# Optimization experiments

Measured on AMD Instinct MI355X. Metric: run time of the kernel, lower is better.

The kernel has to match this reference:

```python
import jax, jax.numpy as jnp
import numpy as np

B = 64          # batch
NV = 256        # n_vert per rod
CS = [256, 256] # cs_n_vert
N = 3 * NV      # num_nodes
RBC = [100, 200]  # rigid_body_coupling_index
HID = 128


def _build_adjacency():
    A = np.zeros((N, N), dtype=np.float32)
    # chain edges: parent rod, child1 rod, child2 rod (hop=1)
    for i in range(NV - 1):
        A[i, i + 1] = 1; A[i + 1, i] = 1
    for i in range(NV, NV + CS[0] - 1):
        A[i, i + 1] = 1; A[i + 1, i] = 1
    for i in range(2 * NV, 2 * NV + CS[1] - 1):
        A[i, i + 1] = 1; A[i + 1, i] = 1
    zero_mask = np.all(A == 0, axis=-1).astype(np.float32)  # (N,)
    A = (A + np.eye(N, dtype=np.float32)) * (1.0 - zero_mask)  # broadcast over columns, as in torch
    # rigid-body coupling edges (asymmetric, faithful to the source)
    for i, r in enumerate(RBC):
        base = NV * (i + 1)
        A[base, r - 1] = 1; A[base, r] = 1; A[base, r + 1] = 1
        if i == 0:
            A[r, NV] = 1; A[r, NV + 1] = 1
        else:
            A[r, NV + CS[i - 1]] = 1; A[r, NV + CS[i - 1] + 1] = 1
    return A


def setup_inputs() -> dict:
    key = jax.random.key(0)
    ks = jax.random.split(key, 10)
    dims = [(6, 2 * HID), (2 * HID, HID), (HID, HID), (HID, 3)]  # gcn1..gcn4
    params = {}
    for li, (fi, fo) in enumerate(dims):
        params[f"W{li+1}"] = jax.random.normal(ks[li], (fo, fi), jnp.float32) / np.sqrt(fi)
        params[f"b{li+1}"] = jnp.zeros((fo,), jnp.float32)
    return {
        "x": jax.random.normal(ks[8], (B, N, 6), jnp.float32),
        "inputs": jax.random.normal(ks[9], (B, N, 3), jnp.float32),
        "adjacency": jnp.asarray(_build_adjacency()),
        **params,
        "parent_sel": jnp.array([0, NV - 1], jnp.int32),
        "child1_sel": jnp.array([NV - 1], jnp.int32),
        "child2_sel": jnp.array([NV - 1], jnp.int32),
    }


def _gcn(A_norm, x, W, b):
    # linear then symmetric-normalized dense aggregation
    return jnp.einsum('ij,bjf->bif', A_norm, x @ W.T + b)


def reference(x, inputs, adjacency, W1, b1, W2, b2, W3, b3, W4, b4,
              parent_sel, child1_sel, child2_sel):
    deg = adjacency.sum(axis=-1)
    deg_safe = jnp.where(deg == 0, 1.0, deg)
    d = jnp.where(deg == 0, 0.0, deg_safe ** -0.5)
    A_norm = adjacency * d[:, None] * d[None, :]

    x4 = x.reshape(B, 3, NV, -1)
    in4 = inputs.reshape(B, 3, NV, 3)
    # clamp input positions (first 3 features) at grasped vertices
    x4 = x4.at[:, 0, parent_sel, 0:3].set(in4[:, 0, parent_sel])
    x4 = x4.at[:, 1, child1_sel, 0:3].set(in4[:, 1, child1_sel])
    x4 = x4.at[:, 2, child2_sel, 0:3].set(in4[:, 2, child2_sel])
    h = x4.reshape(B, N, -1)

    h = jax.nn.relu(_gcn(A_norm, h, W1, b1))
    h = jax.nn.relu(_gcn(A_norm, h, W2, b2))
    h = _gcn(A_norm, h, W3, b3)
    out = _gcn(A_norm, h, W4, b4)

    o4 = out.reshape(B, 3, NV, 3)
    o4 = o4.at[:, 0, parent_sel].set(in4[:, 0, parent_sel])
    o4 = o4.at[:, 1, child1_sel].set(in4[:, 1, child1_sel])
    o4 = o4.at[:, 2, child2_sel].set(in4[:, 2, child2_sel])
    return o4.reshape(B, N, 3)
```

## Files before the change

### kernel.cpp

```cpp
#include <hip/hip_runtime.h>
#include <math.h>

#define B_ 64
#define NV_ 256
#define N_ 768
#define NNZ 8
#define M_ (B_ * N_)

typedef unsigned short us8 __attribute__((ext_vector_type(8)));
typedef unsigned short us4 __attribute__((ext_vector_type(4)));
typedef __bf16 bf16x8 __attribute__((ext_vector_type(8)));
typedef float f32x4 __attribute__((ext_vector_type(4)));

__device__ inline float bf2f(unsigned short u) {
    return __uint_as_float(((unsigned int)u) << 16);
}
__device__ inline unsigned short f2bf(float f) {
    unsigned int u = __float_as_uint(f);
    unsigned int r = u + 0x7fffu + ((u >> 16) & 1u);
    return (unsigned short)(r >> 16);
}
__device__ inline bf16x8 ld_bf8(const unsigned short* p) {
    us8 u = *(const us8*)p;
    return __builtin_bit_cast(bf16x8, u);
}


__global__ __launch_bounds__(256) void k_deg_conv(
    const float* __restrict__ A, const float* __restrict__ W2,
    const float* __restrict__ W3, const int* __restrict__ psel, int np,
    const int* __restrict__ c1, int n1, const int* __restrict__ c2, int n2,
    float* __restrict__ dinv, int* __restrict__ clampf,
    unsigned short* __restrict__ W2b, unsigned short* __restrict__ W3b) {
    int blk = blockIdx.x, tid = threadIdx.x;
    if (blk < 192) {
        int wave = tid >> 6, lane = tid & 63;
        int i = blk * 4 + wave;
        float deg = 0.f;
#pragma unroll
        for (int c0 = 0; c0 < N_; c0 += 64) deg += A[(size_t)i * N_ + c0 + lane];
#pragma unroll
        for (int o = 32; o > 0; o >>= 1) deg += __shfl_xor(deg, o);
        if (lane == 0) dinv[i] = (deg == 0.f) ? 0.f : 1.0f / sqrtf(deg);
    } else if (blk < 384) {
        int idx = (blk - 192) * 256 + tid;
        if (idx < 128 * 256) W2b[idx] = f2bf(W2[idx]);
        else W3b[idx - 128 * 256] = f2bf(W3[idx - 128 * 256]);
    } else {
        clampf[tid] = 0;
        clampf[tid + 256] = 0;
        clampf[tid + 512] = 0;
        __syncthreads();
        if (tid < np) clampf[psel[tid]] = 1;
        else if (tid - np < n1) clampf[NV_ + c1[tid - np]] = 1;
        else if (tid - np - n1 < n2) clampf[2 * NV_ + c2[tid - np - n1]] = 1;
    }
}


__global__ __launch_bounds__(256) void k_sparse(const float* __restrict__ A,
                                                const float* __restrict__ dinv,
                                                int* __restrict__ cols,
                                                float* __restrict__ vals,
                                                float* __restrict__ rowsum) {
    __shared__ int wc[4][NNZ];
    __shared__ float wa[4][NNZ];
    int wave = threadIdx.x >> 6, lane = threadIdx.x & 63;
    int i = blockIdx.x * 4 + wave;
    float di = dinv[i];
    int cnt = 0;
    float rs = 0.f;
#pragma unroll
    for (int c0 = 0; c0 < N_; c0 += 64) {
        int c = c0 + lane;
        float a = A[(size_t)i * N_ + c];
        unsigned long long m = __ballot(a != 0.f);
        if (a != 0.f) {
            float v = a * di * dinv[c];
            int pos = cnt + __popcll(m & ((1ull << lane) - 1ull));
            if (pos < NNZ) {
                wc[wave][pos] = c;
                wa[wave][pos] = v;
            }
            rs += v;
        }
        cnt += (int)__popcll(m);
    }
#pragma unroll
    for (int o = 32; o > 0; o >>= 1) rs += __shfl_xor(rs, o);
    __syncthreads();
    int nn = cnt < NNZ ? cnt : NNZ;
    if (lane < NNZ) {
        int c = (lane < nn) ? wc[wave][lane] : i;
        float v = (lane < nn) ? wa[wave][lane] : 0.f;
        cols[i * NNZ + lane] = c;
        vals[i * NNZ + lane] = v;
    }
    if (lane == 0) rowsum[i] = rs;
}


__global__ __launch_bounds__(256) void k_layer12(
    const float* __restrict__ x, const float* __restrict__ inputs,
    const int* __restrict__ cols, const float* __restrict__ vals,
    const int* __restrict__ clampf, const float* __restrict__ rowsum,
    const float* __restrict__ W1, const float* __restrict__ b1,
    const unsigned short* __restrict__ W2b, const float* __restrict__ b2,
    unsigned short* __restrict__ T2) {
    __shared__ float Xs[64][6];
    __shared__ float W1T[6][256];
    __shared__ float b1s[256];

    int tid = threadIdx.x;
    int blk = blockIdx.x;
    int i0 = (blk % 12) * 64;
    int base = (blk / 12) * N_;
    int wave = tid >> 6, lane = tid & 63;
    int lrow = lane & 15, kgrp = lane >> 4;

    for (int t = tid; t < 1536; t += 256) {
        int k = t >> 8, c = t & 255;
        W1T[k][c] = W1[c * 6 + k];
    }
    b1s[tid] = b1[tid];

    for (int t = lane; t < 96; t += 64) {
        int f = t % 6, ro = t / 6;
        int i = i0 + wave * 16 + ro;
        float s = 0.f;
#pragma unroll
        for (int k = 0; k < NNZ; ++k) {
            int c = cols[i * NNZ + k];
            float v = vals[i * NNZ + k];
            float val = (f < 3 && clampf[c]) ? inputs[(size_t)(base + c) * 3 + f]
                                             : x[(size_t)(base + c) * 6 + f];
            s += v * val;
        }
        Xs[wave * 16 + ro][f] = s;
    }
    __syncthreads();

    int i = i0 + wave * 16 + lrow;
    size_t g = (size_t)(base + i);
    float rs = rowsum[i];
    float xa[6];
#pragma unroll
    for (int k = 0; k < 6; ++k) xa[k] = Xs[wave * 16 + lrow][k];

    f32x4 acc[8];
#pragma unroll
    for (int j = 0; j < 8; ++j) acc[j] = (f32x4){0.f, 0.f, 0.f, 0.f};

#pragma unroll
    for (int s = 0; s < 8; ++s) {
        int c0 = s * 32 + kgrp * 8;
        float h[8];
        f32x4 bv0 = *(const f32x4*)&b1s[c0];
        f32x4 bv1 = *(const f32x4*)&b1s[c0 + 4];
#pragma unroll
        for (int e = 0; e < 4; ++e) {
            h[e] = rs * bv0[e];
            h[4 + e] = rs * bv1[e];
        }
#pragma unroll
        for (int k = 0; k < 6; ++k) {
            f32x4 w0 = *(const f32x4*)&W1T[k][c0];
            f32x4 w1 = *(const f32x4*)&W1T[k][c0 + 4];
#pragma unroll
            for (int e = 0; e < 4; ++e) {
                h[e] += xa[k] * w0[e];
                h[4 + e] += xa[k] * w1[e];
            }
        }
        us8 o;
#pragma unroll
        for (int e = 0; e < 8; ++e) o[e] = f2bf(fmaxf(h[e], 0.f));
        bf16x8 af = __builtin_bit_cast(bf16x8, o);
#pragma unroll
        for (int j = 0; j < 8; ++j) {
            bf16x8 w = ld_bf8(W2b + (size_t)(j * 16 + lrow) * 256 + c0);
            acc[j] = __builtin_amdgcn_mfma_f32_16x16x32_bf16(w, af, acc[j], 0, 0, 0);
        }
    }

#pragma unroll
    for (int j = 0; j < 8; ++j) {
        f32x4 bv = *(const f32x4*)&b2[j * 16 + kgrp * 4];
        us4 o;
#pragma unroll
        for (int e = 0; e < 4; ++e) o[e] = f2bf(acc[j][e] + bv[e]);
        *(us4*)(T2 + g * 128 + j * 16 + kgrp * 4) = o;
    }
}


__global__ __launch_bounds__(256) void k_layer3s(
    const unsigned short* __restrict__ T2, const int* __restrict__ cols,
    const float* __restrict__ vals, const unsigned short* __restrict__ W3b,
    const float* __restrict__ b3, const float* __restrict__ W4,
    float* __restrict__ S) {
    __shared__ float W4s[128 * 3];

    int tid = threadIdx.x;
    int blk = blockIdx.x;
    int i0 = (blk % 12) * 64;
    int base = (blk / 12) * N_;
    int wave = tid >> 6, lane = tid & 63;
    int lrow = lane & 15, kgrp = lane >> 4;

    for (int t = tid; t < 384; t += 256) {
        int d = t % 3, nfeat = t / 3;
        W4s[t] = W4[d * 128 + nfeat];
    }
    __syncthreads();

    int i = i0 + wave * 16 + lrow;
    size_t g = (size_t)(base + i);

    float fa[4][8];
#pragma unroll
    for (int s = 0; s < 4; ++s)
#pragma unroll
        for (int e = 0; e < 8; ++e) fa[s][e] = 0.f;

#pragma unroll
    for (int k = 0; k < NNZ; ++k) {
        int c = cols[i * NNZ + k];
        float v = vals[i * NNZ + k];
        const unsigned short* p = T2 + (size_t)(base + c) * 128 + kgrp * 8;
#pragma unroll
        for (int s = 0; s < 4; ++s) {
            us8 z = *(const us8*)(p + s * 32);
#pragma unroll
            for (int e = 0; e < 8; ++e) fa[s][e] += v * bf2f(z[e]);
        }
    }

    bf16x8 af[4];
#pragma unroll
    for (int s = 0; s < 4; ++s) {
        us8 o;
#pragma unroll
        for (int e = 0; e < 8; ++e) o[e] = f2bf(fmaxf(fa[s][e], 0.f));
        af[s] = __builtin_bit_cast(bf16x8, o);
    }

    f32x4 acc[8];
#pragma unroll
    for (int j = 0; j < 8; ++j) acc[j] = (f32x4){0.f, 0.f, 0.f, 0.f};
#pragma unroll
    for (int s = 0; s < 4; ++s) {
#pragma unroll
        for (int j = 0; j < 8; ++j) {
            bf16x8 w = ld_bf8(W3b + (size_t)(j * 16 + lrow) * 128 + s * 32 + kgrp * 8);
            acc[j] = __builtin_amdgcn_mfma_f32_16x16x32_bf16(w, af[s], acc[j], 0, 0, 0);
        }
    }

    float s0 = 0.f, s1 = 0.f, s2 = 0.f;
#pragma unroll
    for (int j = 0; j < 8; ++j) {
        f32x4 bv = *(const f32x4*)&b3[j * 16 + kgrp * 4];
#pragma unroll
        for (int e = 0; e < 4; ++e) {
            float tv = acc[j][e] + bv[e];
            int nfeat = j * 16 + kgrp * 4 + e;
            s0 += tv * W4s[nfeat * 3 + 0];
            s1 += tv * W4s[nfeat * 3 + 1];
            s2 += tv * W4s[nfeat * 3 + 2];
        }
    }
    s0 += __shfl_xor(s0, 16); s0 += __shfl_xor(s0, 32);
    s1 += __shfl_xor(s1, 16); s1 += __shfl_xor(s1, 32);
    s2 += __shfl_xor(s2, 16); s2 += __shfl_xor(s2, 32);
    if (kgrp == 0) {
        S[g * 3 + 0] = s0;
        S[g * 3 + 1] = s1;
        S[g * 3 + 2] = s2;
    }
}


__global__ __launch_bounds__(256) void k_out2(const float* __restrict__ S,
                                              const float* __restrict__ inputs,
                                              const int* __restrict__ cols,
                                              const float* __restrict__ vals,
                                              const float* __restrict__ rowsum,
                                              const float* __restrict__ b4,
                                              const int* __restrict__ clampf,
                                              float* __restrict__ out) {
    int idx = blockIdx.x * 256 + threadIdx.x;
    if (idx >= M_ * 3) return;
    int f = idx % 3;
    int r = idx / 3;
    int i = r % N_;
    int base = r - i;
    if (clampf[i]) {
        out[idx] = inputs[(size_t)r * 3 + f];
        return;
    }
    float s = rowsum[i] * b4[f];
#pragma unroll
    for (int k = 0; k < NNZ; ++k) {
        int c = cols[i * NNZ + k];
        float vik = vals[i * NNZ + k];
        float u = 0.f;
#pragma unroll
        for (int p = 0; p < NNZ; ++p) {
            int j = cols[c * NNZ + p];
            u += vals[c * NNZ + p] * S[(size_t)(base + j) * 3 + f];
        }
        s += vik * u;
    }
    out[idx] = s;
}


extern "C" void kernel_launch(void* const* d_in, const int* in_sizes, int n_in,
                              void* d_out, int out_size, void* d_ws, size_t ws_size,
                              hipStream_t stream) {
    const float* x      = (const float*)d_in[0];
    const float* inputs = (const float*)d_in[1];
    const float* A      = (const float*)d_in[2];
    const float* W1     = (const float*)d_in[3];
    const float* b1     = (const float*)d_in[4];
    const float* W2     = (const float*)d_in[5];
    const float* b2     = (const float*)d_in[6];
    const float* W3     = (const float*)d_in[7];
    const float* b3     = (const float*)d_in[8];
    const float* W4     = (const float*)d_in[9];
    const float* b4     = (const float*)d_in[10];
    const int* psel     = (const int*)d_in[11];
    const int* c1sel    = (const int*)d_in[12];
    const int* c2sel    = (const int*)d_in[13];
    int np = in_sizes[11], n1 = in_sizes[12], n2 = in_sizes[13];
    float* out = (float*)d_out;

    char* ws = (char*)d_ws;
    float* dinv            = (float*)(ws + 0);
    float* rowsum          = (float*)(ws + 3072);
    int*   clampf          = (int*)(ws + 9216);
    int*   cols            = (int*)(ws + 12288);
    float* vals            = (float*)(ws + 61440);
    unsigned short* W2b    = (unsigned short*)(ws + 110592);
    unsigned short* W3b    = (unsigned short*)(ws + 176128);
    float* S               = (float*)(ws + 417792);
    unsigned short* T2     = (unsigned short*)(ws + 27144192);

    k_deg_conv<<<385, 256, 0, stream>>>(A, W2, W3, psel, np, c1sel, n1, c2sel, n2,
                                        dinv, clampf, W2b, W3b);
    k_sparse<<<192, 256, 0, stream>>>(A, dinv, cols, vals, rowsum);

    k_layer12<<<M_ / 64, 256, 0, stream>>>(x, inputs, cols, vals, clampf, rowsum,
                                           W1, b1, W2b, b2, T2);
    k_layer3s<<<M_ / 64, 256, 0, stream>>>(T2, cols, vals, W3b, b3, W4, S);
    k_out2<<<(M_ * 3 + 255) / 256, 256, 0, stream>>>(S, inputs, cols, vals,
                                                     rowsum, b4, clampf, out);
}
```

Baseline: 75.44 us.

## Fuse all stages into one persistent kernel with grid-wide barriers

Merges the five separate kernel launches into one persistent kernel that walks virtual blocks and separates stages with atomic-counter grid barriers. The degree and sparse-extraction passes are also merged so A is read once, with normalization applied in a later small pass. The aim is to remove launch overhead and inter-kernel gaps. In exchange it adds global-barrier spin costs, a memset launch, and an occupancy query on the host per call. The barrier has a timeout fallback that could silently break correctness if the grid is not fully co-resident.

New measurement: 153.2 us. 2.03x slower.

```diff
diff --git a/kernel.cpp b/kernel.cpp
--- a/kernel.cpp
+++ b/kernel.cpp
@@ -25,335 +25,334 @@
     return __builtin_bit_cast(bf16x8, u);
 }
 
-
-__global__ __launch_bounds__(256) void k_deg_conv(
-    const float* __restrict__ A, const float* __restrict__ W2,
-    const float* __restrict__ W3, const int* __restrict__ psel, int np,
-    const int* __restrict__ c1, int n1, const int* __restrict__ c2, int n2,
-    float* __restrict__ dinv, int* __restrict__ clampf,
-    unsigned short* __restrict__ W2b, unsigned short* __restrict__ W3b) {
-    int blk = blockIdx.x, tid = threadIdx.x;
-    if (blk < 192) {
-        int wave = tid >> 6, lane = tid & 63;
-        int i = blk * 4 + wave;
-        float deg = 0.f;
-#pragma unroll
-        for (int c0 = 0; c0 < N_; c0 += 64) deg += A[(size_t)i * N_ + c0 + lane];
-#pragma unroll
-        for (int o = 32; o > 0; o >>= 1) deg += __shfl_xor(deg, o);
-        if (lane == 0) dinv[i] = (deg == 0.f) ? 0.f : 1.0f / sqrtf(deg);
-    } else if (blk < 384) {
-        int idx = (blk - 192) * 256 + tid;
-        if (idx < 128 * 256) W2b[idx] = f2bf(W2[idx]);
-        else W3b[idx - 128 * 256] = f2bf(W3[idx - 128 * 256]);
-    } else {
-        clampf[tid] = 0;
-        clampf[tid + 256] = 0;
-        clampf[tid + 512] = 0;
-        __syncthreads();
-        if (tid < np) clampf[psel[tid]] = 1;
-        else if (tid - np < n1) clampf[NV_ + c1[tid - np]] = 1;
-        else if (tid - np - n1 < n2) clampf[2 * NV_ + c2[tid - np - n1]] = 1;
-    }
-}
-
-
-__global__ __launch_bounds__(256) void k_sparse(const float* __restrict__ A,
-                                                const float* __restrict__ dinv,
-                                                int* __restrict__ cols,
-                                                float* __restrict__ vals,
-                                                float* __restrict__ rowsum) {
-    __shared__ int wc[4][NNZ];
-    __shared__ float wa[4][NNZ];
-    int wave = threadIdx.x >> 6, lane = threadIdx.x & 63;
-    int i = blockIdx.x * 4 + wave;
-    float di = dinv[i];
-    int cnt = 0;
-    float rs = 0.f;
-#pragma unroll
-    for (int c0 = 0; c0 < N_; c0 += 64) {
-        int c = c0 + lane;
-        float a = A[(size_t)i * N_ + c];
-        unsigned long long m = __ballot(a != 0.f);
-        if (a != 0.f) {
-            float v = a * di * dinv[c];
-            int pos = cnt + __popcll(m & ((1ull << lane) - 1ull));
-            if (pos < NNZ) {
-                wc[wave][pos] = c;
-                wa[wave][pos] = v;
-            }
-            rs += v;
-        }
-        cnt += (int)__popcll(m);
-    }
-#pragma unroll
-    for (int o = 32; o > 0; o >>= 1) rs += __shfl_xor(rs, o);
+struct GP {
+    const float *x, *inputs, *A, *W1, *b1, *W2, *b2, *W3, *b3, *W4, *b4;
+    const int *psel, *c1s, *c2s;
+    int np, n1, n2;
+    float* dinv;
+    float* rowsum;
+    int* clampf;
+    int* cols;
+    float* vals;
+    unsigned short* W2b;
+    unsigned short* W3b;
+    float* S;
+    unsigned short* T2;
+    unsigned int* bar;
+    float* out;
+};
+
+__device__ __forceinline__ void gsync(unsigned int* bar, int slot) {
     __syncthreads();
-    int nn = cnt < NNZ ? cnt : NNZ;
-    if (lane < NNZ) {
-        int c = (lane < nn) ? wc[wave][lane] : i;
-        float v = (lane < nn) ? wa[wave][lane] : 0.f;
-        cols[i * NNZ + lane] = c;
-        vals[i * NNZ + lane] = v;
-    }
-    if (lane == 0) rowsum[i] = rs;
-}
-
-
-__global__ __launch_bounds__(256) void k_layer12(
-    const float* __restrict__ x, const float* __restrict__ inputs,
-    const int* __restrict__ cols, const float* __restrict__ vals,
-    const int* __restrict__ clampf, const float* __restrict__ rowsum,
-    const float* __restrict__ W1, const float* __restrict__ b1,
-    const unsigned short* __restrict__ W2b, const float* __restrict__ b2,
-    unsigned short* __restrict__ T2) {
-    __shared__ float Xs[64][6];
-    __shared__ float W1T[6][256];
-    __shared__ float b1s[256];
-
-    int tid = threadIdx.x;
-    int blk = blockIdx.x;
-    int i0 = (blk % 12) * 64;
-    int base = (blk / 12) * N_;
+    if (threadIdx.x == 0) {
+        __threadfence();
+        atomicAdd(&bar[slot], 1u);
+        unsigned int nb = gridDim.x;
+        long long t0 = clock64();
+        while (atomicAdd(&bar[slot], 0u) < nb) {
+            __builtin_amdgcn_s_sleep(16);
+            if (clock64() - t0 > 200000000LL) break;
+        }
+        __threadfence();
+    }
+    __syncthreads();
+}
+
+__global__ __launch_bounds__(256) void k_mega(GP p) {
+    int tid = threadIdx.x, blk = blockIdx.x;
+    int gd = gridDim.x;
     int wave = tid >> 6, lane = tid & 63;
     int lrow = lane & 15, kgrp = lane >> 4;
 
+    __shared__ union {
+        struct { int wc[4][NNZ]; float wa[4][NNZ]; } sp;
+        struct { float Xs[64][6]; float W1T[6][256]; float b1s[256]; } l12;
+        struct { float W4s[384]; } l3;
+    } sm;
+
+    for (int vb = blk; vb < 385; vb += gd) {
+        if (vb < 192) {
+            int i = vb * 4 + wave;
+            float deg = 0.f;
+            int cnt = 0;
+#pragma unroll
+            for (int c0 = 0; c0 < N_; c0 += 64) {
+                float a = p.A[(size_t)i * N_ + c0 + lane];
+                deg += a;
+                unsigned long long m = __ballot(a != 0.f);
+                if (a != 0.f) {
+                    int pos = cnt + __popcll(m & ((1ull << lane) - 1ull));
+                    if (pos < NNZ) {
+                        sm.sp.wc[wave][pos] = c0 + lane;
+                        sm.sp.wa[wave][pos] = a;
+                    }
+                }
+                cnt += (int)__popcll(m);
+            }
+#pragma unroll
+            for (int o = 32; o > 0; o >>= 1) deg += __shfl_xor(deg, o);
+            __syncthreads();
+            int nn = cnt < NNZ ? cnt : NNZ;
+            if (lane < NNZ) {
+                p.cols[i * NNZ + lane] = (lane < nn) ? sm.sp.wc[wave][lane] : i;
+                p.vals[i * NNZ + lane] = (lane < nn) ? sm.sp.wa[wave][lane] : 0.f;
+            }
+            if (lane == 0) p.dinv[i] = (deg == 0.f) ? 0.f : 1.0f / sqrtf(deg);
+        } else if (vb < 384) {
+            int idx = (vb - 192) * 256 + tid;
+            if (idx < 32768) p.W2b[idx] = f2bf(p.W2[idx]);
+            else p.W3b[idx - 32768] = f2bf(p.W3[idx - 32768]);
+        } else {
+            p.clampf[tid] = 0;
+            p.clampf[tid + 256] = 0;
+            p.clampf[tid + 512] = 0;
+            __syncthreads();
+            if (tid < p.np) p.clampf[p.psel[tid]] = 1;
+            else if (tid - p.np < p.n1) p.clampf[NV_ + p.c1s[tid - p.np]] = 1;
+            else if (tid - p.np - p.n1 < p.n2)
+                p.clampf[2 * NV_ + p.c2s[tid - p.np - p.n1]] = 1;
+        }
+        __syncthreads();
+    }
+    gsync(p.bar, 0);
+
+    for (int idx = blk * 256 + tid; idx < N_ * NNZ; idx += gd * 256) {
+        int i = idx >> 3;
+        int c = p.cols[idx];
+        float v = p.vals[idx] * p.dinv[i] * p.dinv[c];
+        p.vals[idx] = v;
+        float rs = v;
+        rs += __shfl_xor(rs, 1);
+        rs += __shfl_xor(rs, 2);
+        rs += __shfl_xor(rs, 4);
+        if ((idx & 7) == 0) p.rowsum[i] = rs;
+    }
+    gsync(p.bar, 1);
+
     for (int t = tid; t < 1536; t += 256) {
         int k = t >> 8, c = t & 255;
-        W1T[k][c] = W1[c * 6 + k];
-    }
-    b1s[tid] = b1[tid];
-
-    for (int t = lane; t < 96; t += 64) {
-        int f = t % 6, ro = t / 6;
-        int i = i0 + wave * 16 + ro;
-        float s = 0.f;
-#pragma unroll
-        for (int k = 0; k < NNZ; ++k) {
-            int c = cols[i * NNZ + k];
-            float v = vals[i * NNZ + k];
-            float val = (f < 3 && clampf[c]) ? inputs[(size_t)(base + c) * 3 + f]
-                                             : x[(size_t)(base + c) * 6 + f];
-            s += v * val;
-        }
-        Xs[wave * 16 + ro][f] = s;
-    }
-    __syncthreads();
-
-    int i = i0 + wave * 16 + lrow;
-    size_t g = (size_t)(base + i);
-    float rs = rowsum[i];
-    float xa[6];
-#pragma unroll
-    for (int k = 0; k < 6; ++k) xa[k] = Xs[wave * 16 + lrow][k];
-
-    f32x4 acc[8];
-#pragma unroll
-    for (int j = 0; j < 8; ++j) acc[j] = (f32x4){0.f, 0.f, 0.f, 0.f};
-
-#pragma unroll
-    for (int s = 0; s < 8; ++s) {
-        int c0 = s * 32 + kgrp * 8;
-        float h[8];
-        f32x4 bv0 = *(const f32x4*)&b1s[c0];
-        f32x4 bv1 = *(const f32x4*)&b1s[c0 + 4];
-#pragma unroll
-        for (int e = 0; e < 4; ++e) {
-            h[e] = rs * bv0[e];
-            h[4 + e] = rs * bv1[e];
-        }
-#pragma unroll
-        for (int k = 0; k < 6; ++k) {
-            f32x4 w0 = *(const f32x4*)&W1T[k][c0];
-            f32x4 w1 = *(const f32x4*)&W1T[k][c0 + 4];
+        sm.l12.W1T[k][c] = p.W1[c * 6 + k];
+    }
+    sm.l12.b1s[tid] = p.b1[tid];
+
+    for (int vb = blk; vb < 768; vb += gd) {
+        int i0 = (vb % 12) * 64;
+        int base = (vb / 12) * N_;
+        __syncthreads();
+
+        for (int t = lane; t < 96; t += 64) {
+            int f = t % 6, ro = t / 6;
+            int i = i0 + wave * 16 + ro;
+            float s = 0.f;
+#pragma unroll
+            for (int k = 0; k < NNZ; ++k) {
+                int c = p.cols[i * NNZ + k];
+                float v = p.vals[i * NNZ + k];
+                float val = (f < 3 && p.clampf[c]) ? p.inputs[(size_t)(base + c) * 3 + f]
+                                                   : p.x[(size_t)(base + c) * 6 + f];
+                s += v * val;
+            }
+            sm.l12.Xs[wave * 16 + ro][f] = s;
+        }
+        __syncthreads();
+
+        int i = i0 + wave * 16 + lrow;
+        size_t g = (size_t)(base + i);
+        float rs = p.rowsum[i];
+        float xa[6];
+#pragma unroll
+        for (int k = 0; k < 6; ++k) xa[k] = sm.l12.Xs[wave * 16 + lrow][k];
+
+        f32x4 acc[8];
+#pragma unroll
+        for (int j = 0; j < 8; ++j) acc[j] = (f32x4){0.f, 0.f, 0.f, 0.f};
+
+#pragma unroll
+        for (int s = 0; s < 8; ++s) {
+            int c0 = s * 32 + kgrp * 8;
+            float h[8];
+            f32x4 bv0 = *(const f32x4*)&sm.l12.b1s[c0];
+            f32x4 bv1 = *(const f32x4*)&sm.l12.b1s[c0 + 4];
 #pragma unroll
             for (int e = 0; e < 4; ++e) {
-                h[e] += xa[k] * w0[e];
-                h[4 + e] += xa[k] * w1[e];
-            }
-        }
-        us8 o;
-#pragma unroll
-        for (int e = 0; e < 8; ++e) o[e] = f2bf(fmaxf(h[e], 0.f));
-        bf16x8 af = __builtin_bit_cast(bf16x8, o);
+                h[e] = rs * bv0[e];
+                h[4 + e] = rs * bv1[e];
+            }
+#pragma unroll
+            for (int k = 0; k < 6; ++k) {
+                f32x4 w0 = *(const f32x4*)&sm.l12.W1T[k][c0];
+                f32x4 w1 = *(const f32x4*)&sm.l12.W1T[k][c0 + 4];
+#pragma unroll
+                for (int e = 0; e < 4; ++e) {
+                    h[e] += xa[k] * w0[e];
+                    h[4 + e] += xa[k] * w1[e];
+                }
+            }
+            us8 o;
+#pragma unroll
+            for (int e = 0; e < 8; ++e) o[e] = f2bf(fmaxf(h[e], 0.f));
+            bf16x8 af = __builtin_bit_cast(bf16x8, o);
+#pragma unroll
+            for (int j = 0; j < 8; ++j) {
+                bf16x8 w = ld_bf8(p.W2b + (size_t)(j * 16 + lrow) * 256 + c0);
+                acc[j] = __builtin_amdgcn_mfma_f32_16x16x32_bf16(w, af, acc[j], 0, 0, 0);
+            }
+        }
+
 #pragma unroll
         for (int j = 0; j < 8; ++j) {
-            bf16x8 w = ld_bf8(W2b + (size_t)(j * 16 + lrow) * 256 + c0);
-            acc[j] = __builtin_amdgcn_mfma_f32_16x16x32_bf16(w, af, acc[j], 0, 0, 0);
-        }
-    }
-
-#pragma unroll
-    for (int j = 0; j < 8; ++j) {
-        f32x4 bv = *(const f32x4*)&b2[j * 16 + kgrp * 4];
-        us4 o;
-#pragma unroll
-        for (int e = 0; e < 4; ++e) o[e] = f2bf(acc[j][e] + bv[e]);
-        *(us4*)(T2 + g * 128 + j * 16 + kgrp * 4) = o;
-    }
-}
-
-
-__global__ __launch_bounds__(256) void k_layer3s(
-    const unsigned short* __restrict__ T2, const int* __restrict__ cols,
-    const float* __restrict__ vals, const unsigned short* __restrict__ W3b,
-    const float* __restrict__ b3, const float* __restrict__ W4,
-    float* __restrict__ S) {
-    __shared__ float W4s[128 * 3];
-
-    int tid = threadIdx.x;
-    int blk = blockIdx.x;
-    int i0 = (blk % 12) * 64;
-    int base = (blk / 12) * N_;
-    int wave = tid >> 6, lane = tid & 63;
-    int lrow = lane & 15, kgrp = lane >> 4;
+            f32x4 bv = *(const f32x4*)&p.b2[j * 16 + kgrp * 4];
+            us4 o;
+#pragma unroll
+            for (int e = 0; e < 4; ++e) o[e] = f2bf(acc[j][e] + bv[e]);
+            *(us4*)(p.T2 + g * 128 + j * 16 + kgrp * 4) = o;
+        }
+    }
+    gsync(p.bar, 2);
 
     for (int t = tid; t < 384; t += 256) {
         int d = t % 3, nfeat = t / 3;
-        W4s[t] = W4[d * 128 + nfeat];
+        sm.l3.W4s[t] = p.W4[d * 128 + nfeat];
     }
     __syncthreads();
 
-    int i = i0 + wave * 16 + lrow;
-    size_t g = (size_t)(base + i);
-
-    float fa[4][8];
-#pragma unroll
-    for (int s = 0; s < 4; ++s)
-#pragma unroll
-        for (int e = 0; e < 8; ++e) fa[s][e] = 0.f;
-
-#pragma unroll
-    for (int k = 0; k < NNZ; ++k) {
-        int c = cols[i * NNZ + k];
-        float v = vals[i * NNZ + k];
-        const unsigned short* p = T2 + (size_t)(base + c) * 128 + kgrp * 8;
+    for (int vb = blk; vb < 768; vb += gd) {
+        int i0 = (vb % 12) * 64;
+        int base = (vb / 12) * N_;
+        int i = i0 + wave * 16 + lrow;
+        size_t g = (size_t)(base + i);
+
+        float fa[4][8];
+#pragma unroll
+        for (int s = 0; s < 4; ++s)
+#pragma unroll
+            for (int e = 0; e < 8; ++e) fa[s][e] = 0.f;
+
+#pragma unroll
+        for (int k = 0; k < NNZ; ++k) {
+            int c = p.cols[i * NNZ + k];
+            float v = p.vals[i * NNZ + k];
+            const unsigned short* pt = p.T2 + (size_t)(base + c) * 128 + kgrp * 8;
+#pragma unroll
+            for (int s = 0; s < 4; ++s) {
+                us8 z = *(const us8*)(pt + s * 32);
+#pragma unroll
+                for (int e = 0; e < 8; ++e) fa[s][e] += v * bf2f(z[e]);
+            }
+        }
+
+        bf16x8 af[4];
 #pragma unroll
         for (int s = 0; s < 4; ++s) {
-            us8 z = *(const us8*)(p + s * 32);
-#pragma unroll
-            for (int e = 0; e < 8; ++e) fa[s][e] += v * bf2f(z[e]);
-        }
-    }
-
-    bf16x8 af[4];
-#pragma unroll
-    for (int s = 0; s < 4; ++s) {
-        us8 o;
-#pragma unroll
-        for (int e = 0; e < 8; ++e) o[e] = f2bf(fmaxf(fa[s][e], 0.f));
-        af[s] = __builtin_bit_cast(bf16x8, o);
-    }
-
-    f32x4 acc[8];
-#pragma unroll
-    for (int j = 0; j < 8; ++j) acc[j] = (f32x4){0.f, 0.f, 0.f, 0.f};
-#pragma unroll
-    for (int s = 0; s < 4; ++s) {
+            us8 o;
+#pragma unroll
+            for (int e = 0; e < 8; ++e) o[e] = f2bf(fmaxf(fa[s][e], 0.f));
+            af[s] = __builtin_bit_cast(bf16x8, o);
+        }
+
+        f32x4 acc[8];
+#pragma unroll
+        for (int j = 0; j < 8; ++j) acc[j] = (f32x4){0.f, 0.f, 0.f, 0.f};
+#pragma unroll
+        for (int s = 0; s < 4; ++s) {
+#pragma unroll
+            for (int j = 0; j < 8; ++j) {
+                bf16x8 w = ld_bf8(p.W3b + (size_t)(j * 16 + lrow) * 128 + s * 32 + kgrp * 8);
+                acc[j] = __builtin_amdgcn_mfma_f32_16x16x32_bf16(w, af[s], acc[j], 0, 0, 0);
+            }
+        }
+
+        float s0 = 0.f, s1 = 0.f, s2 = 0.f;
 #pragma unroll
         for (int j = 0; j < 8; ++j) {
-            bf16x8 w = ld_bf8(W3b + (size_t)(j * 16 + lrow) * 128 + s * 32 + kgrp * 8);
-            acc[j] = __builtin_amdgcn_mfma_f32_16x16x32_bf16(w, af[s], acc[j], 0, 0, 0);
-        }
-    }
-
-    float s0 = 0.f, s1 = 0.f, s2 = 0.f;
-#pragma unroll
-    for (int j = 0; j < 8; ++j) {
-        f32x4 bv = *(const f32x4*)&b3[j * 16 + kgrp * 4];
-#pragma unroll
-        for (int e = 0; e < 4; ++e) {
-            float tv = acc[j][e] + bv[e];
-            int nfeat = j * 16 + kgrp * 4 + e;
-            s0 += tv * W4s[nfeat * 3 + 0];
-            s1 += tv * W4s[nfeat * 3 + 1];
-            s2 += tv * W4s[nfeat * 3 + 2];
-        }
-    }
-    s0 += __shfl_xor(s0, 16); s0 += __shfl_xor(s0, 32);
-    s1 += __shfl_xor(s1, 16); s1 += __shfl_xor(s1, 32);
-    s2 += __shfl_xor(s2, 16); s2 += __shfl_xor(s2, 32);
-    if (kgrp == 0) {
-        S[g * 3 + 0] = s0;
-        S[g * 3 + 1] = s1;
-        S[g * 3 + 2] = s2;
-    }
-}
-
-
-__global__ __launch_bounds__(256) void k_out2(const float* __restrict__ S,
-                                              const float* __restrict__ inputs,
-                                              const int* __restrict__ cols,
-                                              const float* __restrict__ vals,
-                                              const float* __restrict__ rowsum,
-                                              const float* __restrict__ b4,
-                                              const int* __restrict__ clampf,
-                                              float* __restrict__ out) {
-    int idx = blockIdx.x * 256 + threadIdx.x;
-    if (idx >= M_ * 3) return;
-    int f = idx % 3;
-    int r = idx / 3;
-    int i = r % N_;
-    int base = r - i;
-    if (clampf[i]) {
-        out[idx] = inputs[(size_t)r * 3 + f];
-        return;
-    }
-    float s = rowsum[i] * b4[f];
-#pragma unroll
-    for (int k = 0; k < NNZ; ++k) {
-        int c = cols[i * NNZ + k];
-        float vik = vals[i * NNZ + k];
-        float u = 0.f;
-#pragma unroll
-        for (int p = 0; p < NNZ; ++p) {
-            int j = cols[c * NNZ + p];
-            u += vals[c * NNZ + p] * S[(size_t)(base + j) * 3 + f];
-        }
-        s += vik * u;
-    }
-    out[idx] = s;
+            f32x4 bv = *(const f32x4*)&p.b3[j * 16 + kgrp * 4];
+#pragma unroll
+            for (int e = 0; e < 4; ++e) {
+                float tv = acc[j][e] + bv[e];
+                int nfeat = j * 16 + kgrp * 4 + e;
+                s0 += tv * sm.l3.W4s[nfeat * 3 + 0];
+                s1 += tv * sm.l3.W4s[nfeat * 3 + 1];
+                s2 += tv * sm.l3.W4s[nfeat * 3 + 2];
+            }
+        }
+        s0 += __shfl_xor(s0, 16); s0 += __shfl_xor(s0, 32);
+        s1 += __shfl_xor(s1, 16); s1 += __shfl_xor(s1, 32);
+        s2 += __shfl_xor(s2, 16); s2 += __shfl_xor(s2, 32);
+        if (kgrp == 0) {
+            p.S[g * 3 + 0] = s0;
+            p.S[g * 3 + 1] = s1;
+            p.S[g * 3 + 2] = s2;
+        }
+    }
+    gsync(p.bar, 3);
+
+    for (int idx = blk * 256 + tid; idx < M_ * 3; idx += gd * 256) {
+        int f = idx % 3;
+        int r = idx / 3;
+        int i = r % N_;
+        int base = r - i;
+        if (p.clampf[i]) {
+            p.out[idx] = p.inputs[(size_t)r * 3 + f];
+        } else {
+            float s = p.rowsum[i] * p.b4[f];
+#pragma unroll
+            for (int k = 0; k < NNZ; ++k) {
+                int c = p.cols[i * NNZ + k];
+                float vik = p.vals[i * NNZ + k];
+                float u = 0.f;
+#pragma unroll
+                for (int q = 0; q < NNZ; ++q) {
+                    int j = p.cols[c * NNZ + q];
+                    u += p.vals[c * NNZ + q] * p.S[(size_t)(base + j) * 3 + f];
+                }
+                s += vik * u;
+            }
+            p.out[idx] = s;
+        }
+    }
 }
 
 
 extern "C" void kernel_launch(void* const* d_in, const int* in_sizes, int n_in,
                               void* d_out, int out_size, void* d_ws, size_t ws_size,
                               hipStream_t stream) {
-    const float* x      = (const float*)d_in[0];
-    const float* inputs = (const float*)d_in[1];
-    const float* A      = (const float*)d_in[2];
-    const float* W1     = (const float*)d_in[3];
-    const float* b1     = (const float*)d_in[4];
-    const float* W2     = (const float*)d_in[5];
-    const float* b2     = (const float*)d_in[6];
-    const float* W3     = (const float*)d_in[7];
-    const float* b3     = (const float*)d_in[8];
-    const float* W4     = (const float*)d_in[9];
-    const float* b4     = (const float*)d_in[10];
-    const int* psel     = (const int*)d_in[11];
-    const int* c1sel    = (const int*)d_in[12];
-    const int* c2sel    = (const int*)d_in[13];
-    int np = in_sizes[11], n1 = in_sizes[12], n2 = in_sizes[13];
-    float* out = (float*)d_out;
-
     char* ws = (char*)d_ws;
-    float* dinv            = (float*)(ws + 0);
-    float* rowsum          = (float*)(ws + 3072);
-    int*   clampf          = (int*)(ws + 9216);
-    int*   cols            = (int*)(ws + 12288);
-    float* vals            = (float*)(ws + 61440);
-    unsigned short* W2b    = (unsigned short*)(ws + 110592);
-    unsigned short* W3b    = (unsigned short*)(ws + 176128);
-    float* S               = (float*)(ws + 417792);
-    unsigned short* T2     = (unsigned short*)(ws + 27144192);
-
-    k_deg_conv<<<385, 256, 0, stream>>>(A, W2, W3, psel, np, c1sel, n1, c2sel, n2,
-                                        dinv, clampf, W2b, W3b);
-    k_sparse<<<192, 256, 0, stream>>>(A, dinv, cols, vals, rowsum);
-
-    k_layer12<<<M_ / 64, 256, 0, stream>>>(x, inputs, cols, vals, clampf, rowsum,
-                                           W1, b1, W2b, b2, T2);
-    k_layer3s<<<M_ / 64, 256, 0, stream>>>(T2, cols, vals, W3b, b3, W4, S);
-    k_out2<<<(M_ * 3 + 255) / 256, 256, 0, stream>>>(S, inputs, cols, vals,
-                                                     rowsum, b4, clampf, out);
-}
+    GP p;
+    p.x      = (const float*)d_in[0];
+    p.inputs = (const float*)d_in[1];
+    p.A      = (const float*)d_in[2];
+    p.W1     = (const float*)d_in[3];
+    p.b1     = (const float*)d_in[4];
+    p.W2     = (const float*)d_in[5];
+    p.b2     = (const float*)d_in[6];
+    p.W3     = (const float*)d_in[7];
+    p.b3     = (const float*)d_in[8];
+    p.W4     = (const float*)d_in[9];
+    p.b4     = (const float*)d_in[10];
+    p.psel   = (const int*)d_in[11];
+    p.c1s    = (const int*)d_in[12];
+    p.c2s    = (const int*)d_in[13];
+    p.np = in_sizes[11];
+    p.n1 = in_sizes[12];
+    p.n2 = in_sizes[13];
+    p.dinv   = (float*)(ws + 0);
+    p.rowsum = (float*)(ws + 3072);
+    p.clampf = (int*)(ws + 9216);
+    p.cols   = (int*)(ws + 12288);
+    p.vals   = (float*)(ws + 61440);
+    p.W2b    = (unsigned short*)(ws + 110592);
+    p.W3b    = (unsigned short*)(ws + 176128);
+    p.bar    = (unsigned int*)(ws + 212992);
+    p.S      = (float*)(ws + 417792);
+    p.T2     = (unsigned short*)(ws + 27144192);
+    p.out    = (float*)d_out;
+
+    int bpc = 0;
+    hipError_t e = hipOccupancyMaxActiveBlocksPerMultiprocessor(&bpc, k_mega, 256, 0);
+    if (e != hipSuccess || bpc < 1) bpc = 1;
+    int grid = bpc * 256;
+    if (grid > 768) grid = 768;
+
+    hipMemsetAsync(p.bar, 0, 16, stream);
+    k_mega<<<grid, 256, 0, stream>>>(p);
+}
```

## Fuse layers 1-3 with halo recompute in LDS, split final aggregation

Applied to the files above, without the earlier changes.

Merges the layer-1/2 and layer-3 kernels into one kernel. Each block recomputes layer-2 features for its 64 rows plus a halo of neighbour rows (up to 80 slots) and keeps them in shared memory, so the bf16 T2 intermediate never makes a global round trip. The final two-hop aggregation is split into two one-hop kernels through a small U buffer, which avoids the 64 nested gathers per output. In exchange, halo rows add redundant MFMA work, one wave runs an extra pass, LDS use grows, and there is one more kernel launch. Halo slots are capped at 80, and neighbours beyond that fall back to slot 0.

After: 88.39 us. 1.17x slower.

```diff
diff --git a/kernel.cpp b/kernel.cpp
--- a/kernel.cpp
+++ b/kernel.cpp
@@ -6,6 +6,8 @@
 #define N_ 768
 #define NNZ 8
 #define M_ (B_ * N_)
+#define NH 80
+#define TP 136
 
 typedef unsigned short us8 __attribute__((ext_vector_type(8)));
 typedef unsigned short us4 __attribute__((ext_vector_type(4)));
@@ -44,8 +46,8 @@
         if (lane == 0) dinv[i] = (deg == 0.f) ? 0.f : 1.0f / sqrtf(deg);
     } else if (blk < 384) {
         int idx = (blk - 192) * 256 + tid;
-        if (idx < 128 * 256) W2b[idx] = f2bf(W2[idx]);
-        else W3b[idx - 128 * 256] = f2bf(W3[idx - 128 * 256]);
+        if (idx < 32768) W2b[idx] = f2bf(W2[idx]);
+        else W3b[idx - 32768] = f2bf(W3[idx - 32768]);
     } else {
         clampf[tid] = 0;
         clampf[tid + 256] = 0;
@@ -91,42 +93,76 @@
     __syncthreads();
     int nn = cnt < NNZ ? cnt : NNZ;
     if (lane < NNZ) {
-        int c = (lane < nn) ? wc[wave][lane] : i;
-        float v = (lane < nn) ? wa[wave][lane] : 0.f;
-        cols[i * NNZ + lane] = c;
-        vals[i * NNZ + lane] = v;
+        cols[i * NNZ + lane] = (lane < nn) ? wc[wave][lane] : i;
+        vals[i * NNZ + lane] = (lane < nn) ? wa[wave][lane] : 0.f;
     }
     if (lane == 0) rowsum[i] = rs;
 }
 
 
-__global__ __launch_bounds__(256) void k_layer12(
+__global__ __launch_bounds__(256) void k_l123(
     const float* __restrict__ x, const float* __restrict__ inputs,
     const int* __restrict__ cols, const float* __restrict__ vals,
     const int* __restrict__ clampf, const float* __restrict__ rowsum,
     const float* __restrict__ W1, const float* __restrict__ b1,
     const unsigned short* __restrict__ W2b, const float* __restrict__ b2,
-    unsigned short* __restrict__ T2) {
-    __shared__ float Xs[64][6];
+    const unsigned short* __restrict__ W3b, const float* __restrict__ b3,
+    const float* __restrict__ W4, float* __restrict__ S) {
+    __shared__ unsigned short T2L[NH][TP];
+    __shared__ float Xs[NH][6];
     __shared__ float W1T[6][256];
     __shared__ float b1s[256];
-
-    int tid = threadIdx.x;
-    int blk = blockIdx.x;
+    __shared__ float W4s[384];
+    __shared__ short lmap[N_];
+    __shared__ int ilist[NH];
+    __shared__ int nhs;
+
+    int tid = threadIdx.x, blk = blockIdx.x;
     int i0 = (blk % 12) * 64;
     int base = (blk / 12) * N_;
     int wave = tid >> 6, lane = tid & 63;
     int lrow = lane & 15, kgrp = lane >> 4;
 
+    for (int t = tid; t < N_; t += 256) lmap[t] = -1;
+    if (tid == 0) nhs = 66;
     for (int t = tid; t < 1536; t += 256) {
         int k = t >> 8, c = t & 255;
         W1T[k][c] = W1[c * 6 + k];
     }
     b1s[tid] = b1[tid];
-
-    for (int t = lane; t < 96; t += 64) {
-        int f = t % 6, ro = t / 6;
-        int i = i0 + wave * 16 + ro;
+    for (int t = tid; t < 384; t += 256) {
+        int d = t % 3, nf = t / 3;
+        W4s[t] = W4[d * 128 + nf];
+    }
+    __syncthreads();
+    for (int t = tid; t < 66; t += 256) {
+        int c = i0 - 1 + t;
+        if (c >= 0 && c < N_) {
+            lmap[c] = (short)t;
+            ilist[t] = c;
+        } else {
+            ilist[t] = i0;
+        }
+    }
+    __syncthreads();
+    for (int t = tid; t < 64 * NNZ; t += 256) {
+        int i = i0 + (t >> 3);
+        int c = cols[i * NNZ + (t & 7)];
+        if (lmap[c] < 0) {
+            int slot = atomicAdd(&nhs, 1);
+            if (slot < NH) {
+                lmap[c] = (short)slot;
+                ilist[slot] = c;
+            }
+        }
+    }
+    __syncthreads();
+    int NHs = nhs;
+    if (NHs > NH) NHs = NH;
+
+    for (int t = tid; t < NHs * 6; t += 256) {
+        int sl = t / 6, f = t % 6;
+        int i = ilist[sl];
         float s = 0.f;
 #pragma unroll
         for (int k = 0; k < NNZ; ++k) {
@@ -136,159 +172,170 @@
                                              : x[(size_t)(base + c) * 6 + f];
             s += v * val;
         }
-        Xs[wave * 16 + ro][f] = s;
-    }
-    __syncthreads();
-
-    int i = i0 + wave * 16 + lrow;
-    size_t g = (size_t)(base + i);
-    float rs = rowsum[i];
-    float xa[6];
-#pragma unroll
-    for (int k = 0; k < 6; ++k) xa[k] = Xs[wave * 16 + lrow][k];
-
-    f32x4 acc[8];
-#pragma unroll
-    for (int j = 0; j < 8; ++j) acc[j] = (f32x4){0.f, 0.f, 0.f, 0.f};
-
-#pragma unroll
-    for (int s = 0; s < 8; ++s) {
-        int c0 = s * 32 + kgrp * 8;
-        float h[8];
-        f32x4 bv0 = *(const f32x4*)&b1s[c0];
-        f32x4 bv1 = *(const f32x4*)&b1s[c0 + 4];
-#pragma unroll
-        for (int e = 0; e < 4; ++e) {
-            h[e] = rs * bv0[e];
-            h[4 + e] = rs * bv1[e];
-        }
-#pragma unroll
-        for (int k = 0; k < 6; ++k) {
-            f32x4 w0 = *(const f32x4*)&W1T[k][c0];
-            f32x4 w1 = *(const f32x4*)&W1T[k][c0 + 4];
+        Xs[sl][f] = s;
+    }
+    __syncthreads();
+
+    int npass = (NHs > 64) ? 2 : 1;
+    for (int pass = 0; pass < npass; ++pass) {
+        if (pass == 1 && wave != 0) break;
+        int sl = (pass == 0) ? (wave * 16 + lrow) : (64 + lrow);
+        int act = sl < NHs;
+        int ssl = act ? sl : 0;
+        int i = ilist[ssl];
+        float rs = rowsum[i];
+        float xa[6];
+#pragma unroll
+        for (int k = 0; k < 6; ++k) xa[k] = Xs[ssl][k];
+
+        f32x4 acc[8];
+#pragma unroll
+        for (int j = 0; j < 8; ++j) acc[j] = (f32x4){0.f, 0.f, 0.f, 0.f};
+
+#pragma unroll
+        for (int s = 0; s < 8; ++s) {
+            int c0 = s * 32 + kgrp * 8;
+            float h[8];
+            f32x4 bv0 = *(const f32x4*)&b1s[c0];
+            f32x4 bv1 = *(const f32x4*)&b1s[c0 + 4];
 #pragma unroll
             for (int e = 0; e < 4; ++e) {
-                h[e] += xa[k] * w0[e];
-                h[4 + e] += xa[k] * w1[e];
-            }
-        }
-        us8 o;
-#pragma unroll
-        for (int e = 0; e < 8; ++e) o[e] = f2bf(fmaxf(h[e], 0.f));
-        bf16x8 af = __builtin_bit_cast(bf16x8, o);
+                h[e] = rs * bv0[e];
+                h[4 + e] = rs * bv1[e];
+            }
+#pragma unroll
+            for (int k = 0; k < 6; ++k) {
+                f32x4 w0 = *(const f32x4*)&W1T[k][c0];
+                f32x4 w1 = *(const f32x4*)&W1T[k][c0 + 4];
+#pragma unroll
+                for (int e = 0; e < 4; ++e) {
+                    h[e] += xa[k] * w0[e];
+                    h[4 + e] += xa[k] * w1[e];
+                }
+            }
+            us8 o;
+#pragma unroll
+            for (int e = 0; e < 8; ++e) o[e] = f2bf(fmaxf(h[e], 0.f));
+            bf16x8 af = __builtin_bit_cast(bf16x8, o);
+#pragma unroll
+            for (int j = 0; j < 8; ++j) {
+                bf16x8 w = ld_bf8(W2b + (size_t)(j * 16 + lrow) * 256 + c0);
+                acc[j] = __builtin_amdgcn_mfma_f32_16x16x32_bf16(w, af, acc[j], 0, 0, 0);
+            }
+        }
+
+        if (act) {
+#pragma unroll
+            for (int j = 0; j < 8; ++j) {
+                f32x4 bv = *(const f32x4*)&b2[j * 16 + kgrp * 4];
+                us4 o;
+#pragma unroll
+                for (int e = 0; e < 4; ++e) o[e] = f2bf(acc[j][e] + bv[e]);
+                *(us4*)&T2L[sl][j * 16 + kgrp * 4] = o;
+            }
+        }
+    }
+    __syncthreads();
+
+    {
+        int i = i0 + wave * 16 + lrow;
+        size_t g = (size_t)(base + i);
+
+        float fa[4][8];
+#pragma unroll
+        for (int s = 0; s < 4; ++s)
+#pragma unroll
+            for (int e = 0; e < 8; ++e) fa[s][e] = 0.f;
+
+#pragma unroll
+        for (int k = 0; k < NNZ; ++k) {
+            int c = cols[i * NNZ + k];
+            float v = vals[i * NNZ + k];
+            int sl = lmap[c];
+            if (sl < 0) sl = 0;
+            const unsigned short* pt = &T2L[sl][kgrp * 8];
+#pragma unroll
+            for (int s = 0; s < 4; ++s) {
+                us8 z = *(const us8*)(pt + s * 32);
+#pragma unroll
+                for (int e = 0; e < 8; ++e) fa[s][e] += v * bf2f(z[e]);
+            }
+        }
+
+        bf16x8 af[4];
+#pragma unroll
+        for (int s = 0; s < 4; ++s) {
+            us8 o;
+#pragma unroll
+            for (int e = 0; e < 8; ++e) o[e] = f2bf(fmaxf(fa[s][e], 0.f));
+            af[s] = __builtin_bit_cast(bf16x8, o);
+        }
+
+        f32x4 acc[8];
+#pragma unroll
+        for (int j = 0; j < 8; ++j) acc[j] = (f32x4){0.f, 0.f, 0.f, 0.f};
+#pragma unroll
+        for (int s = 0; s < 4; ++s) {
+#pragma unroll
+            for (int j = 0; j < 8; ++j) {
+                bf16x8 w = ld_bf8(W3b + (size_t)(j * 16 + lrow) * 128 + s * 32 + kgrp * 8);
+                acc[j] = __builtin_amdgcn_mfma_f32_16x16x32_bf16(w, af[s], acc[j], 0, 0, 0);
+            }
+        }
+
+        float s0 = 0.f, s1 = 0.f, s2 = 0.f;
 #pragma unroll
         for (int j = 0; j < 8; ++j) {
-            bf16x8 w = ld_bf8(W2b + (size_t)(j * 16 + lrow) * 256 + c0);
-            acc[j] = __builtin_amdgcn_mfma_f32_16x16x32_bf16(w, af, acc[j], 0, 0, 0);
-        }
-    }
-
-#pragma unroll
-    for (int j = 0; j < 8; ++j) {
-        f32x4 bv = *(const f32x4*)&b2[j * 16 + kgrp * 4];
-        us4 o;
-#pragma unroll
-        for (int e = 0; e < 4; ++e) o[e] = f2bf(acc[j][e] + bv[e]);
-        *(us4*)(T2 + g * 128 + j * 16 + kgrp * 4) = o;
-    }
-}
-
-
-__global__ __launch_bounds__(256) void k_layer3s(
-    const unsigned short* __restrict__ T2, const int* __restrict__ cols,
-    const float* __restrict__ vals, const unsigned short* __restrict__ W3b,
-    const float* __restrict__ b3, const float* __restrict__ W4,
-    float* __restrict__ S) {
-    __shared__ float W4s[128 * 3];
-
-    int tid = threadIdx.x;
-    int blk = blockIdx.x;
-    int i0 = (blk % 12) * 64;
-    int base = (blk / 12) * N_;
-    int wave = tid >> 6, lane = tid & 63;
-    int lrow = lane & 15, kgrp = lane >> 4;
-
-    for (int t = tid; t < 384; t += 256) {
-        int d = t % 3, nfeat = t / 3;
-        W4s[t] = W4[d * 128 + nfeat];
-    }
-    __syncthreads();
-
-    int i = i0 + wave * 16 + lrow;
-    size_t g = (size_t)(base + i);
-
-    float fa[4][8];
-#pragma unroll
-    for (int s = 0; s < 4; ++s)
-#pragma unroll
-        for (int e = 0; e < 8; ++e) fa[s][e] = 0.f;
-
+            f32x4 bv = *(const f32x4*)&b3[j * 16 + kgrp * 4];
+#pragma unroll
+            for (int e = 0; e < 4; ++e) {
+                float tv = acc[j][e] + bv[e];
+                int nf = j * 16 + kgrp * 4 + e;
+                s0 += tv * W4s[nf * 3 + 0];
+                s1 += tv * W4s[nf * 3 + 1];
+                s2 += tv * W4s[nf * 3 + 2];
+            }
+        }
+        s0 += __shfl_xor(s0, 16); s0 += __shfl_xor(s0, 32);
+        s1 += __shfl_xor(s1, 16); s1 += __shfl_xor(s1, 32);
+        s2 += __shfl_xor(s2, 16); s2 += __shfl_xor(s2, 32);
+        if (kgrp == 0) {
+            S[g * 3 + 0] = s0;
+            S[g * 3 + 1] = s1;
+            S[g * 3 + 2] = s2;
+        }
+    }
+}
+
+
+__global__ __launch_bounds__(256) void k_aggS(const float* __restrict__ S,
+                                              const int* __restrict__ cols,
+                                              const float* __restrict__ vals,
+                                              float* __restrict__ U) {
+    int idx = blockIdx.x * 256 + threadIdx.x;
+    if (idx >= M_ * 3) return;
+    int f = idx % 3;
+    int r = idx / 3;
+    int i = r % N_;
+    int base = r - i;
+    float s = 0.f;
 #pragma unroll
     for (int k = 0; k < NNZ; ++k) {
         int c = cols[i * NNZ + k];
-        float v = vals[i * NNZ + k];
-        const unsigned short* p = T2 + (size_t)(base + c) * 128 + kgrp * 8;
-#pragma unroll
-        for (int s = 0; s < 4; ++s) {
-            us8 z = *(const us8*)(p + s * 32);
-#pragma unroll
-            for (int e = 0; e < 8; ++e) fa[s][e] += v * bf2f(z[e]);
-        }
-    }
-
-    bf16x8 af[4];
-#pragma unroll
-    for (int s = 0; s < 4; ++s) {
-        us8 o;
-#pragma unroll
-        for (int e = 0; e < 8; ++e) o[e] = f2bf(fmaxf(fa[s][e], 0.f));
-        af[s] = __builtin_bit_cast(bf16x8, o);
-    }
-
-    f32x4 acc[8];
-#pragma unroll
-    for (int j = 0; j < 8; ++j) acc[j] = (f32x4){0.f, 0.f, 0.f, 0.f};
-#pragma unroll
-    for (int s = 0; s < 4; ++s) {
-#pragma unroll
-        for (int j = 0; j < 8; ++j) {
-            bf16x8 w = ld_bf8(W3b + (size_t)(j * 16 + lrow) * 128 + s * 32 + kgrp * 8);
-            acc[j] = __builtin_amdgcn_mfma_f32_16x16x32_bf16(w, af[s], acc[j], 0, 0, 0);
-        }
-    }
-
-    float s0 = 0.f, s1 = 0.f, s2 = 0.f;
-#pragma unroll
-    for (int j = 0; j < 8; ++j) {
-        f32x4 bv = *(const f32x4*)&b3[j * 16 + kgrp * 4];
-#pragma unroll
-        for (int e = 0; e < 4; ++e) {
-            float tv = acc[j][e] + bv[e];
-            int nfeat = j * 16 + kgrp * 4 + e;
-            s0 += tv * W4s[nfeat * 3 + 0];
-            s1 += tv * W4s[nfeat * 3 + 1];
-            s2 += tv * W4s[nfeat * 3 + 2];
-        }
-    }
-    s0 += __shfl_xor(s0, 16); s0 += __shfl_xor(s0, 32);
-    s1 += __shfl_xor(s1, 16); s1 += __shfl_xor(s1, 32);
-    s2 += __shfl_xor(s2, 16); s2 += __shfl_xor(s2, 32);
-    if (kgrp == 0) {
-        S[g * 3 + 0] = s0;
-        S[g * 3 + 1] = s1;
-        S[g * 3 + 2] = s2;
-    }
-}
-
-
-__global__ __launch_bounds__(256) void k_out2(const float* __restrict__ S,
-                                              const float* __restrict__ inputs,
-                                              const int* __restrict__ cols,
-                                              const float* __restrict__ vals,
-                                              const float* __restrict__ rowsum,
-                                              const float* __restrict__ b4,
-                                              const int* __restrict__ clampf,
-                                              float* __restrict__ out) {
+        s += vals[i * NNZ + k] * S[(size_t)(base + c) * 3 + f];
+    }
+    U[idx] = s;
+}
+
+
+__global__ __launch_bounds__(256) void k_out(const float* __restrict__ U,
+                                             const float* __restrict__ inputs,
+                                             const int* __restrict__ cols,
+                                             const float* __restrict__ vals,
+                                             const float* __restrict__ rowsum,
+                                             const float* __restrict__ b4,
+                                             const int* __restrict__ clampf,
+                                             float* __restrict__ out) {
     int idx = blockIdx.x * 256 + threadIdx.x;
     if (idx >= M_ * 3) return;
     int f = idx % 3;
@@ -303,14 +350,7 @@
 #pragma unroll
     for (int k = 0; k < NNZ; ++k) {
         int c = cols[i * NNZ + k];
-        float vik = vals[i * NNZ + k];
-        float u = 0.f;
-#pragma unroll
-        for (int p = 0; p < NNZ; ++p) {
-            int j = cols[c * NNZ + p];
-            u += vals[c * NNZ + p] * S[(size_t)(base + j) * 3 + f];
-        }
-        s += vik * u;
+        s += vals[i * NNZ + k] * U[(size_t)(base + c) * 3 + f];
     }
     out[idx] = s;
 }
@@ -345,15 +385,15 @@
     unsigned short* W2b    = (unsigned short*)(ws + 110592);
     unsigned short* W3b    = (unsigned short*)(ws + 176128);
     float* S               = (float*)(ws + 417792);
-    unsigned short* T2     = (unsigned short*)(ws + 27144192);
+    float* U               = (float*)(ws + 1048576);
 
     k_deg_conv<<<385, 256, 0, stream>>>(A, W2, W3, psel, np, c1sel, n1, c2sel, n2,
                                         dinv, clampf, W2b, W3b);
     k_sparse<<<192, 256, 0, stream>>>(A, dinv, cols, vals, rowsum);
 
-    k_layer12<<<M_ / 64, 256, 0, stream>>>(x, inputs, cols, vals, clampf, rowsum,
-                                           W1, b1, W2b, b2, T2);
-    k_layer3s<<<M_ / 64, 256, 0, stream>>>(T2, cols, vals, W3b, b3, W4, S);
-    k_out2<<<(M_ * 3 + 255) / 256, 256, 0, stream>>>(S, inputs, cols, vals,
-                                                     rowsum, b4, clampf, out);
-}
+    k_l123<<<768, 256, 0, stream>>>(x, inputs, cols, vals, clampf, rowsum,
+                                    W1, b1, W2b, b2, W3b, b3, W4, S);
+    k_aggS<<<(M_ * 3 + 255) / 256, 256, 0, stream>>>(S, cols, vals, U);
+    k_out<<<(M_ * 3 + 255) / 256, 256, 0, stream>>>(U, inputs, cols, vals,
+                                                    rowsum, b4, clampf, out);
+}
```
